# Kernel tuning notes

Measured on AMD Instinct MI355X. Metric: run time of the kernel, lower is better.

## Reference

```python
import jax, jax.numpy as jnp
import numpy as np

B, H_IMG, W_IMG, DIM, HEADS, WS = 8, 56, 56, 768, 12, 14
SEQ = H_IMG * W_IMG
HEAD_DIM = DIM // HEADS
MLP_HID = 4 * DIM
SCALE = HEAD_DIM ** -0.5


def setup_inputs() -> dict:
    key = jax.random.key(0)
    ks = jax.random.split(key, 8)
    s = 0.02
    return {
        "x": jax.random.normal(ks[0], (B, SEQ, DIM), jnp.float32),
        "ln1_scale": jnp.ones((DIM,), jnp.float32),
        "ln1_bias": jnp.zeros((DIM,), jnp.float32),
        "qkv_w": jax.random.normal(ks[1], (DIM, 3 * DIM), jnp.float32) * s,
        "qkv_b": jnp.zeros((3 * DIM,), jnp.float32),
        "rel_pos_h": jax.random.normal(ks[2], (2 * WS - 1, HEAD_DIM), jnp.float32) * s,
        "rel_pos_w": jax.random.normal(ks[3], (2 * WS - 1, HEAD_DIM), jnp.float32) * s,
        "proj_w": jax.random.normal(ks[4], (DIM, DIM), jnp.float32) * s,
        "proj_b": jnp.zeros((DIM,), jnp.float32),
        "ln2_scale": jnp.ones((DIM,), jnp.float32),
        "ln2_bias": jnp.zeros((DIM,), jnp.float32),
        "fc1_w": jax.random.normal(ks[5], (DIM, MLP_HID), jnp.float32) * s,
        "fc1_b": jnp.zeros((MLP_HID,), jnp.float32),
        "fc2_w": jax.random.normal(ks[6], (MLP_HID, DIM), jnp.float32) * s,
        "fc2_b": jnp.zeros((DIM,), jnp.float32),
        "H": H_IMG,
        "W": W_IMG,
    }


def _layernorm(x, scale, bias, eps=1e-5):
    mu = x.mean(-1, keepdims=True)
    var = x.var(-1, keepdims=True)
    return (x - mu) / jnp.sqrt(var + eps) * scale + bias


def _window_attn(x, H, W, qkv_w, qkv_b, rel_pos_h, rel_pos_w, proj_w, proj_b):
    # x: (B, H*W, C); H, W divisible by WS so the torch pad branch is a no-op
    Bn, N, C = x.shape
    nh, nw = H // WS, W // WS
    # window_partition: (B, H, W, C) -> (B*nh*nw, WS*WS, C)
    xw = (x.reshape(Bn, nh, WS, nw, WS, C)
            .transpose(0, 1, 3, 2, 4, 5)
            .reshape(-1, WS * WS, C))
    Bw, Nw = xw.shape[0], WS * WS
    qkv = (xw @ qkv_w + qkv_b).reshape(Bw, Nw, 3, HEADS, HEAD_DIM).transpose(2, 0, 3, 1, 4)
    q = qkv[0] * SCALE  # scaled q also used for rel-pos terms (matches torch)
    k, v = qkv[1], qkv[2]
    attn = jnp.einsum('bhnd,bhmd->bhnm', q, k)  # (Bw, heads, Nw, Nw)
    # relative position bias (q_shape == k_shape == (WS, WS), ratios == 1)
    dist = jnp.arange(WS)[:, None] - jnp.arange(WS)[None, :] + (WS - 1)
    Rh = rel_pos_h[dist]  # (WS, WS, head_dim)
    Rw = rel_pos_w[dist]
    r_q = q.reshape(Bw, HEADS, WS, WS, HEAD_DIM)
    rel_h = jnp.einsum('byhwc,hkc->byhwk', r_q, Rh)
    rel_w = jnp.einsum('byhwc,wkc->byhwk', r_q, Rw)
    attn = (attn.reshape(Bw, HEADS, WS, WS, WS, WS)
            + rel_h[:, :, :, :, :, None]
            + rel_w[:, :, :, :, None, :]).reshape(Bw, HEADS, Nw, Nw)
    attn = jax.nn.softmax(attn, axis=-1)
    out = jnp.einsum('bhnm,bhmd->bhnd', attn, v).transpose(0, 2, 1, 3).reshape(Bw, Nw, C)
    out = out @ proj_w + proj_b
    # window_reverse: (Bw, WS*WS, C) -> (B, H*W, C)
    out = (out.reshape(Bn, nh, nw, WS, WS, C)
              .transpose(0, 1, 3, 2, 4, 5)
              .reshape(Bn, H * W, C))
    return out


def reference(x, ln1_scale, ln1_bias, qkv_w, qkv_b, rel_pos_h, rel_pos_w,
              proj_w, proj_b, ln2_scale, ln2_bias, fc1_w, fc1_b, fc2_w, fc2_b, H, W):
    a = _window_attn(_layernorm(x, ln1_scale, ln1_bias), H, W,
                     qkv_w, qkv_b, rel_pos_h, rel_pos_w, proj_w, proj_b)
    x = x + a
    h = _layernorm(x, ln2_scale, ln2_bias)
    h = jax.nn.gelu(h @ fc1_w + fc1_b, approximate=False)  # torch nn.GELU is exact erf
    x = x + (h @ fc2_w + fc2_b)
    return x
```

## Files before the change

kernel.cpp:

```cpp
#include <hip/hip_runtime.h>
#include <stdint.h>

typedef unsigned short u16;
typedef __bf16 bf16x8 __attribute__((ext_vector_type(8)));
typedef float f32x4 __attribute__((ext_vector_type(4)));
typedef unsigned uint32x4 __attribute__((ext_vector_type(4)));
typedef unsigned uint32x2 __attribute__((ext_vector_type(2)));

#define DEVI __device__ __forceinline__

static constexpr int DIM = 768;
static constexpr int SEQL = 3136;
static constexpr int MROWS = 25088;
static constexpr int HEADS = 12;
static constexpr int HD = 64;
static constexpr int NW = 196;
static constexpr float QSCALE = 0.125f;
static constexpr int ATTN_SMEM = 72704;
static constexpr int GEMM_SMEM = 49152;

DEVI float b2f(u16 u) { union { unsigned i; float f; } v; v.i = ((unsigned)u) << 16; return v.f; }
DEVI u16 f2b(float f) { union { float f; unsigned u; } v; v.f = f; return (u16)((v.u + 0x7FFFu + ((v.u >> 16) & 1u)) >> 16); }
DEVI unsigned pack2(float a, float b) { return (unsigned)f2b(a) | ((unsigned)f2b(b) << 16); }
DEVI bf16x8 u4bf(uint4 u) { union { uint4 a; bf16x8 b; } c; c.a = u; return c.b; }

DEVI float gelu_f(float x) {
  float x2 = x * x;
  float y = x * (1.5957691216f + 0.0713548162726f * x2);
  float e = __expf(-y);
  return x * __builtin_amdgcn_rcpf(1.f + e);
}

DEVI void gl_lds16(const void* g, void* l) {
  __builtin_amdgcn_global_load_lds((const __attribute__((address_space(1))) void*)g,
                                   (__attribute__((address_space(3))) void*)l, 16, 0, 0);
}

DEVI bf16x8 ldg_b8(const u16* p) {
  union { uint4 u; bf16x8 v; } r;
  const uint2* p2 = (const uint2*)p;
  uint2 lo = p2[0], hi = p2[1];
  r.u.x = lo.x; r.u.y = lo.y; r.u.z = hi.x; r.u.w = hi.y;
  return r.v;
}

__global__ __launch_bounds__(256) void pack_b(const float* __restrict__ in,
                                              u16* __restrict__ out, int K, int N) {
  int f8 = blockIdx.x * 256 + threadIdx.x;
  int l = f8 & 63;
  int rest = f8 >> 6;
  int s = rest & 1, nf = (rest >> 1) & 3, wn2 = (rest >> 3) & 1, kt = rest >> 4;
  int bn = blockIdx.y;
  int n = bn * 128 + wn2 * 64 + nf * 16 + (l & 15);
  int kb = kt * 64 + s * 32 + (l >> 4) * 8;
  size_t obase = (((size_t)bn * (K >> 6) + kt) * 2 + wn2) * 4096 + (nf * 2 + s) * 512 + (size_t)l * 8;
  #pragma unroll
  for (int e = 0; e < 8; ++e)
    out[obase + e] = f2b(in[(size_t)(kb + e) * N + n]);
}

__global__ __launch_bounds__(256) void cvt_rpb(const float* __restrict__ rph,
                                               const float* __restrict__ rpw,
                                               u16* __restrict__ rpb) {
  int i = blockIdx.x * 256 + threadIdx.x;
  int tbl = i >> 11, r = (i >> 6) & 31, c = i & 63;
  float v = (r < 27) ? (tbl ? rpw : rph)[r * 64 + c] : 0.f;
  rpb[i] = f2b(v);
}

template<bool REMAP>
__global__ __launch_bounds__(256) void ln_kernel(const float* __restrict__ xin,
                                                 const float* __restrict__ g,
                                                 const float* __restrict__ bb,
                                                 u16* __restrict__ outw) {
  const int l = threadIdx.x & 63, w = threadIdx.x >> 6;
  const int r = blockIdx.x * 4 + w;
  const float* xr = xin + (size_t)r * DIM;
  f32x4 v[3], gv[3], bv[3];
  #pragma unroll
  for (int j = 0; j < 3; ++j) {
    v[j]  = *(const f32x4*)(xr + j * 256 + l * 4);
    gv[j] = *(const f32x4*)(g  + j * 256 + l * 4);
    bv[j] = *(const f32x4*)(bb + j * 256 + l * 4);
  }
  float s1 = 0.f, s2 = 0.f;
  #pragma unroll
  for (int j = 0; j < 3; ++j)
    #pragma unroll
    for (int e = 0; e < 4; ++e) { s1 += v[j][e]; s2 += v[j][e] * v[j][e]; }
  #pragma unroll
  for (int o = 1; o < 64; o <<= 1) { s1 += __shfl_xor(s1, o); s2 += __shfl_xor(s2, o); }
  float mean = s1 * (1.f / 768.f);
  float var = s2 * (1.f / 768.f) - mean * mean;
  float rstd = rsqrtf(var + 1e-5f);
  size_t orow;
  if constexpr (REMAP) {
    int b = r / SEQL, s = r % SEQL;
    int h = s / 56, ww = s % 56;
    orow = (size_t)(b * 16 + (h / 14) * 4 + (ww / 14)) * NW + (h % 14) * 14 + (ww % 14);
  } else {
    orow = (size_t)r;
  }
  u16* orp = outw + orow * DIM;
  #pragma unroll
  for (int j = 0; j < 3; ++j) {
    uint2 o2;
    o2.x = pack2((v[j][0] - mean) * rstd * gv[j][0] + bv[j][0],
                 (v[j][1] - mean) * rstd * gv[j][1] + bv[j][1]);
    o2.y = pack2((v[j][2] - mean) * rstd * gv[j][2] + bv[j][2],
                 (v[j][3] - mean) * rstd * gv[j][3] + bv[j][3]);
    *(uint2*)(orp + j * 256 + l * 4) = o2;
  }
}

struct Epi {
  const float* bias;
  const float* x;
  float* outf;
  u16* q; u16* k; u16* v;
  u16* o16;
};

#define MFMA_BF16 __builtin_amdgcn_mfma_f32_16x16x32_bf16

template<int K, int N, int EPI>
__global__ __launch_bounds__(256, 3)
void gemm6_ep(const u16* __restrict__ A, const u16* __restrict__ Bp, Epi ep) {
  extern __shared__ __align__(16) char gsm[];

  constexpr int NBN = N / 128;
  constexpr int NSTC = NBN / 6;
  constexpr int NKT = K / 64;

  const int tid = threadIdx.x;
  const int l = tid & 63, w = tid >> 6;
  const int lr = l & 15, lg = l >> 4;

  const int nwg = gridDim.x;
  const int cpx = nwg >> 3;
  const int wg = (blockIdx.x & 7) * cpx + (blockIdx.x >> 3);
  const int st = wg / 42, r42 = wg - st * 42;
  const int bm = (st / NSTC) * 7 + r42 / 6;
  const int bn = (st - (st / NSTC) * NSTC) * 6 + r42 - (r42 / 6) * 6;
  const int wm = (w >> 1) * 64, wn = (w & 1) * 64;

  const u16* Ab = A + (size_t)bm * 128 * K;
  const u16* Bw = Bp + (((size_t)bn * NKT) * 2 + (w & 1)) * 4096 + (size_t)l * 8;

  int srcoff[4];
  #pragma unroll
  for (int p = 0; p < 4; ++p) {
    int si = p * 256 + tid;
    int row = si >> 3;
    srcoff[p] = row * K + (((si & 7) ^ (row & 7)) << 3);
  }
  #define STG(kt, buf) do {                                                     \
    char* _d = gsm + (buf) * 16384;                                             \
    _Pragma("unroll")                                                           \
    for (int _p = 0; _p < 4; ++_p)                                              \
      gl_lds16(Ab + srcoff[_p] + (size_t)(kt) * 64, _d + _p * 4096 + tid * 16); \
  } while (0)

  const int p0 = lg ^ (lr & 7);
  const int p1 = p0 ^ 4;

  f32x4 zero4 = {0.f, 0.f, 0.f, 0.f};
  f32x4 acc[4][4];
  #pragma unroll
  for (int i = 0; i < 4; ++i)
    #pragma unroll
    for (int j = 0; j < 4; ++j) acc[i][j] = zero4;

  STG(0, 0);
  STG(1, 1);

  for (int t = 0; t < NKT; ++t) {
    if (t + 1 < NKT) asm volatile("s_waitcnt vmcnt(4)" ::: "memory");
    else             asm volatile("s_waitcnt vmcnt(0)" ::: "memory");
    __builtin_amdgcn_s_barrier();

    uint4 braw[4][2];
    const u16* bt = Bw + (size_t)t * 8192;
    #pragma unroll
    for (int nf = 0; nf < 4; ++nf)
      #pragma unroll
      for (int s = 0; s < 2; ++s)
        braw[nf][s] = *(const uint4*)(bt + (nf * 2 + s) * 512);

    if (t + 2 < NKT) STG(t + 2, (t + 2) % 3);

    const u16* cA = (const u16*)(gsm + (t % 3) * 16384);
    bf16x8 af[4][2];
    #pragma unroll
    for (int mf = 0; mf < 4; ++mf) {
      af[mf][0] = *(const bf16x8*)(cA + (wm + mf * 16 + lr) * 64 + p0 * 8);
      af[mf][1] = *(const bf16x8*)(cA + (wm + mf * 16 + lr) * 64 + p1 * 8);
    }
    __builtin_amdgcn_s_setprio(1);
    #pragma unroll
    for (int mf = 0; mf < 4; ++mf)
      #pragma unroll
      for (int nf = 0; nf < 4; ++nf) {
        acc[mf][nf] = MFMA_BF16(af[mf][0], u4bf(braw[nf][0]), acc[mf][nf], 0, 0, 0);
        acc[mf][nf] = MFMA_BF16(af[mf][1], u4bf(braw[nf][1]), acc[mf][nf], 0, 0, 0);
      }
    __builtin_amdgcn_s_setprio(0);
  }
  #undef STG

  __syncthreads();
  float* tp = (float*)(gsm + w * 8448);
  const int ccl = (l & 3) * 16;
  const int cbase = bn * 128 + wn + ccl;
  const int col0 = bn * 128 + wn;
  f32x4 bs[4];
  #pragma unroll
  for (int jj = 0; jj < 4; ++jj) bs[jj] = *(const f32x4*)(ep.bias + cbase + jj * 4);

  const bool isV = (EPI == 0) && (col0 >= 2 * DIM);
  const float bvl = ep.bias[col0 + l];
  const int vhead = (col0 - 2 * DIM) >> 6;

  #pragma unroll
  for (int q = 0; q < 2; ++q) {
    if (q == 1) { asm volatile("s_waitcnt lgkmcnt(0)" ::: "memory"); __builtin_amdgcn_sched_barrier(0); }
    #pragma unroll
    for (int mf2 = 0; mf2 < 2; ++mf2)
      #pragma unroll
      for (int nf = 0; nf < 4; ++nf)
        #pragma unroll
        for (int e = 0; e < 4; ++e)
          tp[(mf2 * 16 + lg * 4 + e) * 66 + nf * 16 + lr] = acc[q * 2 + mf2][nf][e];
    asm volatile("s_waitcnt lgkmcnt(0)" ::: "memory");
    __builtin_amdgcn_sched_barrier(0);

    if (isV) {
      #pragma unroll
      for (int gidx = 0; gidx < 2; ++gidx) {
        const int row0 = bm * 128 + wm + q * 32 + gidx * 16;
        const int win0 = row0 / NW;
        const int win15 = (row0 + 15) / NW;
        float vx[16];
        #pragma unroll
        for (int i = 0; i < 16; ++i)
          vx[i] = tp[(gidx * 16 + i) * 66 + l] + bvl;
        if (win0 == win15) {
          const int pos0 = row0 - win0 * NW;
          u16* dst = ep.v + ((size_t)(win0 * HEADS + vhead) * HD + l) * NW + pos0;
          #pragma unroll
          for (int jj = 0; jj < 4; ++jj) {
            uint32x2 o2;
            o2[0] = pack2(vx[jj * 4 + 0], vx[jj * 4 + 1]);
            o2[1] = pack2(vx[jj * 4 + 2], vx[jj * 4 + 3]);
            __builtin_nontemporal_store(o2, (uint32x2*)(dst + jj * 4));
          }
        } else {
          #pragma unroll
          for (int i = 0; i < 16; ++i) {
            int row = row0 + i;
            int win = row / NW, pos = row - win * NW;
            __builtin_nontemporal_store(f2b(vx[i]),
                ep.v + ((size_t)(win * HEADS + vhead) * HD + l) * NW + pos);
          }
        }
      }
      continue;
    }

    #pragma unroll
    for (int pp = 0; pp < 2; ++pp) {
      const int rowl = pp * 16 + (l >> 2);
      const int r = bm * 128 + wm + q * 32 + rowl;
      const int c = cbase;
      f32x4 vv[4];
      #pragma unroll
      for (int jj = 0; jj < 4; ++jj) {
        #pragma unroll
        for (int j2 = 0; j2 < 4; ++j2)
          vv[jj][j2] = tp[rowl * 66 + ccl + jj * 4 + j2];
        vv[jj] += bs[jj];
      }

      if constexpr (EPI == 0) {
        const int which = c / DIM;
        const int hdc = c - which * DIM;
        const int head = hdc >> 6, d0 = hdc & 63;
        const int win = r / NW, pos = r - win * NW;
        const size_t wh = (size_t)win * HEADS + head;
        if (which == 0) {
          uint32x4 o0, o1;
          o0[0] = pack2(vv[0][0] * QSCALE, vv[0][1] * QSCALE);
          o0[1] = pack2(vv[0][2] * QSCALE, vv[0][3] * QSCALE);
          o0[2] = pack2(vv[1][0] * QSCALE, vv[1][1] * QSCALE);
          o0[3] = pack2(vv[1][2] * QSCALE, vv[1][3] * QSCALE);
          o1[0] = pack2(vv[2][0] * QSCALE, vv[2][1] * QSCALE);
          o1[1] = pack2(vv[2][2] * QSCALE, vv[2][3] * QSCALE);
          o1[2] = pack2(vv[3][0] * QSCALE, vv[3][1] * QSCALE);
          o1[3] = pack2(vv[3][2] * QSCALE, vv[3][3] * QSCALE);
          u16* dst = ep.q + (wh * NW + pos) * HD + d0;
          __builtin_nontemporal_store(o0, (uint32x4*)dst);
          __builtin_nontemporal_store(o1, (uint32x4*)(dst + 8));
        } else {
          uint32x4 o0, o1;
          o0[0] = pack2(vv[0][0], vv[0][1]); o0[1] = pack2(vv[0][2], vv[0][3]);
          o0[2] = pack2(vv[1][0], vv[1][1]); o0[3] = pack2(vv[1][2], vv[1][3]);
          o1[0] = pack2(vv[2][0], vv[2][1]); o1[1] = pack2(vv[2][2], vv[2][3]);
          o1[2] = pack2(vv[3][0], vv[3][1]); o1[3] = pack2(vv[3][2], vv[3][3]);
          u16* dst = ep.k + (wh * NW + pos) * HD + d0;
          __builtin_nontemporal_store(o0, (uint32x4*)dst);
          __builtin_nontemporal_store(o1, (uint32x4*)(dst + 8));
        }
      } else if constexpr (EPI == 1) {
        const int win = r / NW, pos = r - win * NW;
        const int b = win >> 4, wi = win & 15;
        const int hh = (wi >> 2) * 14 + pos / 14;
        const int ww2 = (wi & 3) * 14 + pos % 14;
        const size_t orow = (size_t)b * SEQL + hh * 56 + ww2;
        const f32x4* px = (const f32x4*)(ep.x + orow * DIM + c);
        f32x4* po = (f32x4*)(ep.outf + orow * DIM + c);
        #pragma unroll
        for (int jj = 0; jj < 4; ++jj) {
          f32x4 t2 = px[jj] + vv[jj];
          __builtin_nontemporal_store(t2, po + jj);
        }
      } else if constexpr (EPI == 2) {
        float gg[16];
        #pragma unroll
        for (int jj = 0; jj < 4; ++jj)
          #pragma unroll
          for (int j2 = 0; j2 < 4; ++j2)
            gg[jj * 4 + j2] = gelu_f(vv[jj][j2]);
        uint32x4 o0, o1;
        o0[0] = pack2(gg[0], gg[1]);   o0[1] = pack2(gg[2], gg[3]);
        o0[2] = pack2(gg[4], gg[5]);   o0[3] = pack2(gg[6], gg[7]);
        o1[0] = pack2(gg[8], gg[9]);   o1[1] = pack2(gg[10], gg[11]);
        o1[2] = pack2(gg[12], gg[13]); o1[3] = pack2(gg[14], gg[15]);
        u16* dst = ep.o16 + (size_t)r * N + c;
        __builtin_nontemporal_store(o0, (uint32x4*)dst);
        __builtin_nontemporal_store(o1, (uint32x4*)(dst + 8));
      } else {
        f32x4* po = (f32x4*)(ep.outf + (size_t)r * N + c);
        #pragma unroll
        for (int jj = 0; jj < 4; ++jj) {
          f32x4 t2 = po[jj] + vv[jj];
          __builtin_nontemporal_store(t2, po + jj);
        }
      }
    }
  }
}

__global__ __launch_bounds__(256, 2)
void attn_kernel(const u16* __restrict__ qbuf, const u16* __restrict__ kbuf,
                 const u16* __restrict__ vt, const u16* __restrict__ rpb,
                 u16* __restrict__ abuf) {
  extern __shared__ __align__(16) char smem[];
  u16* sK = (u16*)smem;
  u16* sP = (u16*)(smem + 26624);
  float* sT = (float*)(smem + 56320);

  const int tid = threadIdx.x;
  const int l = tid & 63, w = tid >> 6;
  const int lr = l & 15, lg = l >> 4;
  const int wh = blockIdx.x;
  const int win = wh / HEADS, head = wh - win * HEADS;

  const u16* Qg = qbuf + (size_t)wh * (NW * HD);
  const u16* Kg = kbuf + (size_t)wh * (NW * HD);
  const u16* Vg = vt + (size_t)wh * (HD * NW);

  for (int t = tid; t < 1664; t += 256) {
    int r8 = t >> 3, c8 = t & 7;
    int s = (t & ~7) | (c8 ^ (r8 & 7));
    if (s >= 1568) s &= 1023;
    gl_lds16(Kg + s * 8, (char*)sK + t * 16);
  }
  __syncthreads();

  f32x4 zero4 = {0.f, 0.f, 0.f, 0.f};
  u16* myP = sP + w * (16 * 232);
  float* myT = sT + w * (16 * 64);

  for (int c = 0; c < 4; ++c) {
    const int chunk = w + 4 * c;
    if (chunk > 12) break;

    int qrow = chunk * 16 + lr; if (qrow > 195) qrow = 195;
    bf16x8 aq0 = *(const bf16x8*)(Qg + (size_t)qrow * HD + lg * 8);
    bf16x8 aq1 = *(const bf16x8*)(Qg + (size_t)qrow * HD + 32 + lg * 8);

    f32x4 th[2], tw[2];
    #pragma unroll
    for (int nf2 = 0; nf2 < 2; ++nf2) {
      const u16* bh = rpb + (nf2 * 16 + lr) * 64;
      const u16* bw = rpb + 2048 + (nf2 * 16 + lr) * 64;
      f32x4 a = zero4, b = zero4;
      a = MFMA_BF16(aq0, *(const bf16x8*)(bh + lg * 8), a, 0, 0, 0);
      a = MFMA_BF16(aq1, *(const bf16x8*)(bh + 32 + lg * 8), a, 0, 0, 0);
      b = MFMA_BF16(aq0, *(const bf16x8*)(bw + lg * 8), b, 0, 0, 0);
      b = MFMA_BF16(aq1, *(const bf16x8*)(bw + 32 + lg * 8), b, 0, 0, 0);
      th[nf2] = a; tw[nf2] = b;
    }
    #pragma unroll
    for (int nf2 = 0; nf2 < 2; ++nf2)
      #pragma unroll
      for (int e = 0; e < 4; ++e) {
        myT[(lg * 4 + e) * 64 + nf2 * 16 + lr]      = th[nf2][e];
        myT[(lg * 4 + e) * 64 + 32 + nf2 * 16 + lr] = tw[nf2][e];
      }

    f32x4 accs[13];
    #pragma unroll
    for (int nf = 0; nf < 13; ++nf) {
      int krow = nf * 16 + lr;
      int ksw = (krow & 7) << 3;
      bf16x8 b0 = *(const bf16x8*)(sK + krow * 64 + ((lg * 8) ^ ksw));
      bf16x8 b1 = *(const bf16x8*)(sK + krow * 64 + ((32 + lg * 8) ^ ksw));
      f32x4 cc = zero4;
      cc = MFMA_BF16(aq0, b0, cc, 0, 0, 0);
      cc = MFMA_BF16(aq1, b1, cc, 0, 0, 0);
      accs[nf] = cc;
    }

    int ihv[4], iwv[4];
    #pragma unroll
    for (int e = 0; e < 4; ++e) {
      int gi = chunk * 16 + lg * 4 + e;
      ihv[e] = (gi * 9363) >> 17;
      iwv[e] = gi - ihv[e] * 14;
    }
    float mrow[4] = {-3e38f, -3e38f, -3e38f, -3e38f};
    #pragma unroll
    for (int nf = 0; nf < 13; ++nf) {
      int j = nf * 16 + lr;
      int jh = (j * 9363) >> 17;
      int jw = j - jh * 14;
      #pragma unroll
      for (int e = 0; e < 4; ++e) {
        int ic = lg * 4 + e;
        float s = accs[nf][e]
                + myT[ic * 64 + ((ihv[e] - jh + 13) & 63)]
                + myT[ic * 64 + 32 + (iwv[e] - jw + 13)];
        if (nf == 12 && lr >= 4) s = -1e30f;
        accs[nf][e] = s;
        mrow[e] = fmaxf(mrow[e], s);
      }
    }
    #pragma unroll
    for (int e = 0; e < 4; ++e) {
      float v = mrow[e];
      v = fmaxf(v, __shfl_xor(v, 1)); v = fmaxf(v, __shfl_xor(v, 2));
      v = fmaxf(v, __shfl_xor(v, 4)); v = fmaxf(v, __shfl_xor(v, 8));
      mrow[e] = v;
    }
    float ssum[4] = {0.f, 0.f, 0.f, 0.f};
    #pragma unroll
    for (int nf = 0; nf < 13; ++nf)
      #pragma unroll
      for (int e = 0; e < 4; ++e) {
        float p = __expf(accs[nf][e] - mrow[e]);
        accs[nf][e] = p;
        ssum[e] += p;
      }
    #pragma unroll
    for (int e = 0; e < 4; ++e) {
      float v = ssum[e];
      v += __shfl_xor(v, 1); v += __shfl_xor(v, 2);
      v += __shfl_xor(v, 4); v += __shfl_xor(v, 8);
      ssum[e] = 1.f / v;
    }
    #pragma unroll
    for (int nf = 0; nf < 13; ++nf)
      #pragma unroll
      for (int e = 0; e < 4; ++e)
        myP[(lg * 4 + e) * 232 + nf * 16 + lr] = f2b(accs[nf][e] * ssum[e]);
    #pragma unroll
    for (int e = 0; e < 4; ++e)
      myP[(lg * 4 + e) * 232 + 208 + lr] = 0;

    f32x4 acco[4];
    #pragma unroll
    for (int nf = 0; nf < 4; ++nf) acco[nf] = zero4;
    #pragma unroll
    for (int ks = 0; ks < 7; ++ks) {
      bf16x8 ap = *(const bf16x8*)(myP + lr * 232 + ks * 32 + lg * 8);
      #pragma unroll
      for (int nf = 0; nf < 4; ++nf) {
        bf16x8 bv = ldg_b8(Vg + (size_t)(nf * 16 + lr) * NW + ks * 32 + lg * 8);
        acco[nf] = MFMA_BF16(ap, bv, acco[nf], 0, 0, 0);
      }
    }
    u16* ob = abuf + (size_t)win * NW * DIM + head * HD;
    #pragma unroll
    for (int nf = 0; nf < 4; ++nf)
      #pragma unroll
      for (int e = 0; e < 4; ++e) {
        int row = chunk * 16 + lg * 4 + e;
        if (row < 196) ob[(size_t)row * DIM + nf * 16 + lr] = f2b(acco[nf][e]);
      }
  }
}

extern "C" void kernel_launch(void* const* d_in, const int* in_sizes, int n_in,
                              void* d_out, int out_size, void* d_ws, size_t ws_size,
                              hipStream_t stream) {
  (void)in_sizes; (void)n_in; (void)out_size; (void)ws_size;
  const float* x    = (const float*)d_in[0];
  const float* ln1s = (const float*)d_in[1];
  const float* ln1b = (const float*)d_in[2];
  const float* qkvw = (const float*)d_in[3];
  const float* qkvb = (const float*)d_in[4];
  const float* rph  = (const float*)d_in[5];
  const float* rpw  = (const float*)d_in[6];
  const float* pjw  = (const float*)d_in[7];
  const float* pjb  = (const float*)d_in[8];
  const float* ln2s = (const float*)d_in[9];
  const float* ln2b = (const float*)d_in[10];
  const float* f1w  = (const float*)d_in[11];
  const float* f1b  = (const float*)d_in[12];
  const float* f2w  = (const float*)d_in[13];
  const float* f2b_ = (const float*)d_in[14];
  float* out = (float*)d_out;

  char* ws = (char*)d_ws;
  u16* qkvwT = (u16*)ws;
  u16* projwT = qkvwT + 1769472;
  u16* fc1wT  = qkvwT + 2359296;
  u16* fc2wT  = qkvwT + 4718592;
  u16* xw   = (u16*)(ws + 14155776);
  u16* qbuf = (u16*)(ws + 52690944);
  u16* kbuf = qbuf + 19267584;
  u16* vtb  = kbuf + 19267584;
  u16* h2   = (u16*)(ws + 168296448);
  u16* abuf = xw;
  u16* h1   = xw;
  u16* rpb  = h2;

  (void)hipFuncSetAttribute((const void*)attn_kernel,
                            hipFuncAttributeMaxDynamicSharedMemorySize, ATTN_SMEM);
  (void)hipFuncSetAttribute((const void*)gemm6_ep<768, 2304, 0>,
                            hipFuncAttributeMaxDynamicSharedMemorySize, GEMM_SMEM);
  (void)hipFuncSetAttribute((const void*)gemm6_ep<768, 768, 1>,
                            hipFuncAttributeMaxDynamicSharedMemorySize, GEMM_SMEM);
  (void)hipFuncSetAttribute((const void*)gemm6_ep<768, 3072, 2>,
                            hipFuncAttributeMaxDynamicSharedMemorySize, GEMM_SMEM);
  (void)hipFuncSetAttribute((const void*)gemm6_ep<3072, 768, 3>,
                            hipFuncAttributeMaxDynamicSharedMemorySize, GEMM_SMEM);

  pack_b<<<dim3(768 / 16, 2304 / 128), 256, 0, stream>>>(qkvw, qkvwT, 768, 2304);
  pack_b<<<dim3(768 / 16, 768 / 128),  256, 0, stream>>>(pjw, projwT, 768, 768);
  pack_b<<<dim3(768 / 16, 3072 / 128), 256, 0, stream>>>(f1w, fc1wT, 768, 3072);
  pack_b<<<dim3(3072 / 16, 768 / 128), 256, 0, stream>>>(f2w, fc2wT, 3072, 768);
  cvt_rpb<<<16, 256, 0, stream>>>(rph, rpw, rpb);

  ln_kernel<true><<<MROWS / 4, 256, 0, stream>>>(x, ln1s, ln1b, xw);

  { Epi e{}; e.bias = qkvb; e.q = qbuf; e.k = kbuf; e.v = vtb;
    gemm6_ep<768, 2304, 0><<<196 * 18, 256, GEMM_SMEM, stream>>>(xw, qkvwT, e); }

  attn_kernel<<<1536, 256, ATTN_SMEM, stream>>>(qbuf, kbuf, vtb, rpb, abuf);

  { Epi e{}; e.bias = pjb; e.x = x; e.outf = out;
    gemm6_ep<768, 768, 1><<<196 * 6, 256, GEMM_SMEM, stream>>>(abuf, projwT, e); }

  ln_kernel<false><<<MROWS / 4, 256, 0, stream>>>(out, ln2s, ln2b, h2);

  { Epi e{}; e.bias = f1b; e.o16 = h1;
    gemm6_ep<768, 3072, 2><<<196 * 24, 256, GEMM_SMEM, stream>>>(h2, fc1wT, e); }

  { Epi e{}; e.bias = f2b_; e.outf = out;
    gemm6_ep<3072, 768, 3><<<196 * 6, 256, GEMM_SMEM, stream>>>(h1, fc2wT, e); }
}
```

Baseline: 852.3 us.

## Merge weight-packing launches into one kernel and simplify V store epilogue

Combines the four weight-packing launches and the rel-pos conversion into a single prep kernel dispatched by block index, to cut launch overhead. It also drops the dedicated V-tile epilogue that used LDS-transposed, vectorized stores. V now goes through the generic per-row path with scalar strided bf16 stores. This simplifies the code but may make V writes less coalesced.

```diff
diff --git a/kernel.cpp b/kernel.cpp
--- a/kernel.cpp
+++ b/kernel.cpp
@@ -5,7 +5,6 @@
 typedef __bf16 bf16x8 __attribute__((ext_vector_type(8)));
 typedef float f32x4 __attribute__((ext_vector_type(4)));
 typedef unsigned uint32x4 __attribute__((ext_vector_type(4)));
-typedef unsigned uint32x2 __attribute__((ext_vector_type(2)));
 
 #define DEVI __device__ __forceinline__
 
@@ -44,13 +43,12 @@
   return r.v;
 }
 
-__global__ __launch_bounds__(256) void pack_b(const float* __restrict__ in,
-                                              u16* __restrict__ out, int K, int N) {
-  int f8 = blockIdx.x * 256 + threadIdx.x;
+DEVI void pack_body(const float* __restrict__ in, u16* __restrict__ out,
+                    int K, int N, int xb, int bn, int tid) {
+  int f8 = xb * 256 + tid;
   int l = f8 & 63;
   int rest = f8 >> 6;
   int s = rest & 1, nf = (rest >> 1) & 3, wn2 = (rest >> 3) & 1, kt = rest >> 4;
-  int bn = blockIdx.y;
   int n = bn * 128 + wn2 * 64 + nf * 16 + (l & 15);
   int kb = kt * 64 + s * 32 + (l >> 4) * 8;
   size_t obase = (((size_t)bn * (K >> 6) + kt) * 2 + wn2) * 4096 + (nf * 2 + s) * 512 + (size_t)l * 8;
@@ -59,13 +57,28 @@
     out[obase + e] = f2b(in[(size_t)(kb + e) * N + n]);
 }
 
-__global__ __launch_bounds__(256) void cvt_rpb(const float* __restrict__ rph,
-                                               const float* __restrict__ rpw,
-                                               u16* __restrict__ rpb) {
-  int i = blockIdx.x * 256 + threadIdx.x;
-  int tbl = i >> 11, r = (i >> 6) & 31, c = i & 63;
-  float v = (r < 27) ? (tbl ? rpw : rph)[r * 64 + c] : 0.f;
-  rpb[i] = f2b(v);
+__global__ __launch_bounds__(256)
+void prep_all(const float* __restrict__ qkvw, const float* __restrict__ pjw,
+              const float* __restrict__ f1w, const float* __restrict__ f2w,
+              const float* __restrict__ rph, const float* __restrict__ rpw,
+              u16* __restrict__ qkvwT, u16* __restrict__ projwT,
+              u16* __restrict__ fc1wT, u16* __restrict__ fc2wT,
+              u16* __restrict__ rpb) {
+  const int bid = blockIdx.x, tid = threadIdx.x;
+  if (bid < 864) {
+    pack_body(qkvw, qkvwT, 768, 2304, bid % 48, bid / 48, tid);
+  } else if (bid < 1152) {
+    int r = bid - 864;  pack_body(pjw, projwT, 768, 768, r % 48, r / 48, tid);
+  } else if (bid < 2304) {
+    int r = bid - 1152; pack_body(f1w, fc1wT, 768, 3072, r % 48, r / 48, tid);
+  } else if (bid < 3456) {
+    int r = bid - 2304; pack_body(f2w, fc2wT, 3072, 768, r % 192, r / 192, tid);
+  } else {
+    int i = (bid - 3456) * 256 + tid;
+    int tbl = i >> 11, r = (i >> 6) & 31, c = i & 63;
+    float v = (r < 27) ? (tbl ? rpw : rph)[r * 64 + c] : 0.f;
+    rpb[i] = f2b(v);
+  }
 }
 
 template<bool REMAP>
@@ -212,14 +225,9 @@
   float* tp = (float*)(gsm + w * 8448);
   const int ccl = (l & 3) * 16;
   const int cbase = bn * 128 + wn + ccl;
-  const int col0 = bn * 128 + wn;
   f32x4 bs[4];
   #pragma unroll
   for (int jj = 0; jj < 4; ++jj) bs[jj] = *(const f32x4*)(ep.bias + cbase + jj * 4);
-
-  const bool isV = (EPI == 0) && (col0 >= 2 * DIM);
-  const float bvl = ep.bias[col0 + l];
-  const int vhead = (col0 - 2 * DIM) >> 6;
 
   #pragma unroll
   for (int q = 0; q < 2; ++q) {
@@ -233,39 +241,6 @@
           tp[(mf2 * 16 + lg * 4 + e) * 66 + nf * 16 + lr] = acc[q * 2 + mf2][nf][e];
     asm volatile("s_waitcnt lgkmcnt(0)" ::: "memory");
     __builtin_amdgcn_sched_barrier(0);
-
-    if (isV) {
-      #pragma unroll
-      for (int gidx = 0; gidx < 2; ++gidx) {
-        const int row0 = bm * 128 + wm + q * 32 + gidx * 16;
-        const int win0 = row0 / NW;
-        const int win15 = (row0 + 15) / NW;
-        float vx[16];
-        #pragma unroll
-        for (int i = 0; i < 16; ++i)
-          vx[i] = tp[(gidx * 16 + i) * 66 + l] + bvl;
-        if (win0 == win15) {
-          const int pos0 = row0 - win0 * NW;
-          u16* dst = ep.v + ((size_t)(win0 * HEADS + vhead) * HD + l) * NW + pos0;
-          #pragma unroll
-          for (int jj = 0; jj < 4; ++jj) {
-            uint32x2 o2;
-            o2[0] = pack2(vx[jj * 4 + 0], vx[jj * 4 + 1]);
-            o2[1] = pack2(vx[jj * 4 + 2], vx[jj * 4 + 3]);
-            __builtin_nontemporal_store(o2, (uint32x2*)(dst + jj * 4));
-          }
-        } else {
-          #pragma unroll
-          for (int i = 0; i < 16; ++i) {
-            int row = row0 + i;
-            int win = row / NW, pos = row - win * NW;
-            __builtin_nontemporal_store(f2b(vx[i]),
-                ep.v + ((size_t)(win * HEADS + vhead) * HD + l) * NW + pos);
-          }
-        }
-      }
-      continue;
-    }
 
     #pragma unroll
     for (int pp = 0; pp < 2; ++pp) {
@@ -300,7 +275,7 @@
           u16* dst = ep.q + (wh * NW + pos) * HD + d0;
           __builtin_nontemporal_store(o0, (uint32x4*)dst);
           __builtin_nontemporal_store(o1, (uint32x4*)(dst + 8));
-        } else {
+        } else if (which == 1) {
           uint32x4 o0, o1;
           o0[0] = pack2(vv[0][0], vv[0][1]); o0[1] = pack2(vv[0][2], vv[0][3]);
           o0[2] = pack2(vv[1][0], vv[1][1]); o0[3] = pack2(vv[1][2], vv[1][3]);
@@ -309,6 +284,13 @@
           u16* dst = ep.k + (wh * NW + pos) * HD + d0;
           __builtin_nontemporal_store(o0, (uint32x4*)dst);
           __builtin_nontemporal_store(o1, (uint32x4*)(dst + 8));
+        } else {
+          #pragma unroll
+          for (int jj = 0; jj < 4; ++jj)
+            #pragma unroll
+            for (int j2 = 0; j2 < 4; ++j2)
+              __builtin_nontemporal_store(f2b(vv[jj][j2]),
+                  ep.v + (wh * HD + d0 + jj * 4 + j2) * NW + pos);
         }
       } else if constexpr (EPI == 1) {
         const int win = r / NW, pos = r - win * NW;
@@ -547,11 +529,8 @@
   (void)hipFuncSetAttribute((const void*)gemm6_ep<3072, 768, 3>,
                             hipFuncAttributeMaxDynamicSharedMemorySize, GEMM_SMEM);
 
-  pack_b<<<dim3(768 / 16, 2304 / 128), 256, 0, stream>>>(qkvw, qkvwT, 768, 2304);
-  pack_b<<<dim3(768 / 16, 768 / 128),  256, 0, stream>>>(pjw, projwT, 768, 768);
-  pack_b<<<dim3(768 / 16, 3072 / 128), 256, 0, stream>>>(f1w, fc1wT, 768, 3072);
-  pack_b<<<dim3(3072 / 16, 768 / 128), 256, 0, stream>>>(f2w, fc2wT, 3072, 768);
-  cvt_rpb<<<16, 256, 0, stream>>>(rph, rpw, rpb);
+  prep_all<<<3472, 256, 0, stream>>>(qkvw, pjw, f1w, f2w, rph, rpw,
+                                     qkvwT, projwT, fc1wT, fc2wT, rpb);
 
   ln_kernel<true><<<MROWS / 4, 256, 0, stream>>>(x, ln1s, ln1b, xw);
 
```

Result: faster. 769.6 us (-9.7%).
